# Kernel tuning notes

Measured on AMD Instinct MI355X. Metric: run time of the kernel, lower is better.

Reference implementation:

```python
import jax, jax.numpy as jnp
import numpy as np

NUM_EMB = 1024
EMB_DIM = 256
BETA = 0.25


def setup_inputs() -> dict:
    key = jax.random.key(0)
    k1, k2 = jax.random.split(key)
    z_e = jax.random.normal(k1, (32, EMB_DIM, 32, 32), dtype=jnp.float32)
    # original inits uniform(-1/num_emb, 1/num_emb)
    emb_weight = jax.random.uniform(k2, (NUM_EMB, EMB_DIM), dtype=jnp.float32,
                                    minval=-1.0 / NUM_EMB, maxval=1.0 / NUM_EMB)
    return {"z_e": z_e, "emb_weight": emb_weight}


def reference(z_e, emb_weight):
    # (B, C, H, W) -> (B, H, W, C)
    z = jnp.transpose(z_e, (0, 2, 3, 1))
    B, H, W, C = z.shape
    z_flat = z.reshape(-1, C)  # (N, C)
    # squared L2 distances to codebook: ||z||^2 + ||e||^2 - 2 z e^T
    d = (jnp.sum(z_flat ** 2, axis=1, keepdims=True)
         + jnp.sum(emb_weight ** 2, axis=1)
         - 2.0 * jnp.matmul(z_flat, emb_weight.T))  # (N, num_emb)
    encoding_indices = jnp.argmin(d, axis=1)  # (N,)
    # one-hot matmul == gather of codebook rows
    z_q = jnp.take(emb_weight, encoding_indices, axis=0).reshape(B, H, W, C)
    # vq losses
    L_e = jnp.mean((jax.lax.stop_gradient(z_q) - z) ** 2)
    L_q = jnp.mean((z_q - jax.lax.stop_gradient(z)) ** 2)
    vq_loss = L_e + BETA * L_q
    # straight-through estimator
    z_q_st = z + jax.lax.stop_gradient(z_q - z)
    z_q_out = jnp.transpose(z_q_st, (0, 3, 1, 2))  # (B, C, H, W)
    return z_q_out, vq_loss, encoding_indices
```

## Files before the change

kernel.cpp:

```cpp
#include <hip/hip_runtime.h>

#define NUM_EMB 1024
#define EMB_DIM 256
#define NPIX    32768
#define HW      1024
#define ZQ_ELEMS 8388608

#define WS_TNORM 8
#define WS_SNORM 8192
#define WS_KEYS  139264
#define WS_CNT   401408
#define WS_EB    403456

typedef unsigned long long u64;
typedef unsigned int u32;
typedef unsigned short u16;

typedef __bf16 bf16x8 __attribute__((ext_vector_type(8)));
typedef float f32x16 __attribute__((ext_vector_type(16)));
typedef u16 u16x8 __attribute__((ext_vector_type(8)));

__device__ __forceinline__ size_t eb_idx(int p, int g, int kt, int ks, int hi,
                                         int cl) {
  return ((((((size_t)p * 32 + g) * 8 + kt) * 2 + ks) * 2 + hi) * 32 + cl) * 8;
}

__device__ __forceinline__ float pw128_sq(const float* x, int stride) {
  float r[8];
#pragma unroll
  for (int j = 0; j < 8; ++j) {
    float v = x[(size_t)j * stride];
    r[j] = __fmul_rn(v, v);
  }
  for (int i = 8; i < 128; i += 8) {
#pragma unroll
    for (int j = 0; j < 8; ++j) {
      float v = x[(size_t)(i + j) * stride];
      r[j] = __fadd_rn(r[j], __fmul_rn(v, v));
    }
  }
  float s01 = __fadd_rn(r[0], r[1]);
  float s23 = __fadd_rn(r[2], r[3]);
  float s45 = __fadd_rn(r[4], r[5]);
  float s67 = __fadd_rn(r[6], r[7]);
  return __fadd_rn(__fadd_rn(s01, s23), __fadd_rn(s45, s67));
}

__device__ __forceinline__ void split3(float x, u16& h, u16& m, u16& l) {
  u32 u = __float_as_uint(x);
  u16 hb = (u16)((u + 0x7fffu + ((u >> 16) & 1u)) >> 16);
  float hf = __uint_as_float((u32)hb << 16);
  float r1 = x - hf;
  u32 u1 = __float_as_uint(r1);
  u16 mb = (u16)((u1 + 0x7fffu + ((u1 >> 16) & 1u)) >> 16);
  float mf = __uint_as_float((u32)mb << 16);
  float r2 = r1 - mf;
  u32 u2 = __float_as_uint(r2);
  u16 lb = (u16)((u2 + 0x7fffu + ((u2 >> 16) & 1u)) >> 16);
  h = hb; m = mb; l = lb;
}

__device__ __forceinline__ u64 shfl_xor_u64(u64 v, int msk) {
  const u32 lo = __shfl_xor((u32)v, msk, 64);
  const u32 hi = __shfl_xor((u32)(v >> 32), msk, 64);
  return ((u64)hi << 32) | lo;
}

__global__ __launch_bounds__(256) void vq_prep_kernel(
    const float* __restrict__ z, const float* __restrict__ emb,
    float* __restrict__ tnorm, float* __restrict__ snorm,
    u64* __restrict__ keys, double* __restrict__ loss_accum,
    u32* __restrict__ counter, u16* __restrict__ EB) {
  const int gid = blockIdx.x * 256 + threadIdx.x;
  if (gid == 0) *loss_accum = 0.0;
  if (gid == 1) *counter = 0u;
  if (gid < NPIX) {
    keys[gid] = ~0ull;
    const int b = gid >> 10, hw = gid & 1023;
    const float* base = z + (size_t)b * (EMB_DIM * HW) + hw;
    snorm[gid] = __fadd_rn(pw128_sq(base, HW), pw128_sq(base + (size_t)128 * HW, HW));
  } else {
    const int k = gid - NPIX;
    if (k < NUM_EMB) {
      const float* row = emb + (size_t)k * EMB_DIM;
      tnorm[k] = __fadd_rn(pw128_sq(row, 1), pw128_sq(row + 128, 1));
      const int g = k >> 5, cl = k & 31;
      for (int c = 0; c < EMB_DIM; c += 8) {
        u16x8 vh, vm, vl;
#pragma unroll
        for (int j = 0; j < 8; ++j) {
          u16 h_, m_, l_;
          split3(row[c + j], h_, m_, l_);
          vh[j] = h_; vm[j] = m_; vl[j] = l_;
        }
        const int kt = c >> 5, ks = (c >> 4) & 1, hi = (c >> 3) & 1;
        *(u16x8*)(EB + eb_idx(0, g, kt, ks, hi, cl)) = vh;
        *(u16x8*)(EB + eb_idx(1, g, kt, ks, hi, cl)) = vm;
        *(u16x8*)(EB + eb_idx(2, g, kt, ks, hi, cl)) = vl;
      }
    }
  }
}

__global__ __launch_bounds__(256, 2) void vq_main_kernel(
    const float* __restrict__ z, const u16* __restrict__ EB,
    const float* __restrict__ tnorm, const float* __restrict__ snorm,
    u64* __restrict__ keys) {
  __shared__ __align__(16) u16 zs[4][3][64][40];
  __shared__ u64 part[128][2];

  const int t   = threadIdx.x;
  const int hb  = blockIdx.x;
  const int bid = (hb & 7) * 256 + (hb >> 3);
  const int pt  = bid >> 3;
  const int ntb = bid & 7;
  const int m0  = pt * 128;
  const int n0  = ntb * 128;
  const int b   = m0 >> 10;
  const int hw0 = m0 & 1023;

  const int l    = t & 63;
  const int wid  = t >> 6;
  const int wpx0 = (wid >> 1) * 64;
  const int wcb  = (wid & 1) * 64;
  const int cl   = l & 31;
  const int hi   = l >> 5;
  const int gb   = ntb * 4 + (wid & 1) * 2;

  const int m_ = l & 31;
  const int h_ = l >> 5;
  const float* zcol = z + (size_t)b * (EMB_DIM * HW) + hw0 + wpx0 + 2 * m_;

  float2 gz[16];
  bf16x8 geA[3][2], geB[3][2];

  auto load_gz = [&](int kt) {
#pragma unroll
    for (int j = 0; j < 16; ++j)
      gz[j] = *(const float2*)(zcol + (size_t)(kt * 32 + h_ * 16 + j) * HW);
  };
  auto load_ge = [&](bf16x8 dst[3][2], int kt, int ks) {
#pragma unroll
    for (int p = 0; p < 3; ++p)
#pragma unroll
      for (int nn = 0; nn < 2; ++nn)
        dst[p][nn] = *(const bf16x8*)(EB + eb_idx(p, gb + nn, kt, ks, hi, cl));
  };
  auto stage = [&]() {
#pragma unroll
    for (int r = 0; r < 2; ++r) {
#pragma unroll
      for (int c = 0; c < 2; ++c) {
        u16x8 vh, vm, vl;
#pragma unroll
        for (int j = 0; j < 8; ++j) {
          const float x = r ? gz[c * 8 + j].y : gz[c * 8 + j].x;
          u16 h3, m3, l3;
          split3(x, h3, m3, l3);
          vh[j] = h3; vm[j] = m3; vl[j] = l3;
        }
        *(u16x8*)&zs[wid][0][2 * m_ + r][h_ * 16 + c * 8] = vh;
        *(u16x8*)&zs[wid][1][2 * m_ + r][h_ * 16 + c * 8] = vm;
        *(u16x8*)&zs[wid][2][2 * m_ + r][h_ * 16 + c * 8] = vl;
      }
    }
  };

  f32x16 acc[2][2];
#pragma unroll
  for (int i = 0; i < 2; ++i)
#pragma unroll
    for (int j = 0; j < 2; ++j)
#pragma unroll
      for (int r = 0; r < 16; ++r) acc[i][j][r] = 0.0f;

  load_gz(0);
  load_ge(geA, 0, 0);
  stage();
  load_gz(1);

  for (int kt = 0; kt < 8; ++kt) {
    load_ge(geB, kt, 1);
    {
      bf16x8 af[3][2];
#pragma unroll
      for (int p = 0; p < 3; ++p)
#pragma unroll
        for (int mt = 0; mt < 2; ++mt)
          af[p][mt] = *(const bf16x8*)&zs[wid][p][mt * 32 + cl][hi * 8];
#define PROD(PA, PB, GE)                                                      \
      _Pragma("unroll")                                                       \
      for (int mt = 0; mt < 2; ++mt) {                                        \
        _Pragma("unroll")                                                     \
        for (int nn = 0; nn < 2; ++nn)                                        \
          acc[mt][nn] = __builtin_amdgcn_mfma_f32_32x32x16_bf16(              \
              af[PA][mt], GE[PB][nn], acc[mt][nn], 0, 0, 0);                  \
      }
      PROD(0, 0, geA)
      PROD(0, 1, geA)
      PROD(1, 0, geA)
      PROD(1, 1, geA)
      PROD(0, 2, geA)
      PROD(2, 0, geA)
    }
    if (kt < 7) load_ge(geA, kt + 1, 0);
    {
      bf16x8 af[3][2];
#pragma unroll
      for (int p = 0; p < 3; ++p)
#pragma unroll
        for (int mt = 0; mt < 2; ++mt)
          af[p][mt] = *(const bf16x8*)&zs[wid][p][mt * 32 + cl][16 + hi * 8];
      PROD(0, 0, geB)
      PROD(0, 1, geB)
      PROD(1, 0, geB)
      PROD(1, 1, geB)
      PROD(0, 2, geB)
      PROD(2, 0, geB)
#undef PROD
    }
    if (kt < 7) {
      stage();
      if (kt < 6) load_gz(kt + 2);
    }
  }

  const float tv0 = tnorm[n0 + wcb + cl];
  const float tv1 = tnorm[n0 + wcb + 32 + cl];
  u64 bk[2][16];
#pragma unroll
  for (int mt = 0; mt < 2; ++mt)
#pragma unroll
    for (int reg = 0; reg < 16; ++reg) {
      const int row = wpx0 + mt * 32 + (reg & 3) + 8 * (reg >> 2) + 4 * hi;
      const float s = snorm[m0 + row];
      const float d0 = __fsub_rn(__fadd_rn(s, tv0), 2.0f * acc[mt][0][reg]);
      const float d1 = __fsub_rn(__fadd_rn(s, tv1), 2.0f * acc[mt][1][reg]);
      const u64 k0 = ((u64)__float_as_uint(d0) << 32) | (u32)(n0 + wcb + cl);
      const u64 k1 =
          ((u64)__float_as_uint(d1) << 32) | (u32)(n0 + wcb + 32 + cl);
      bk[mt][reg] = k0 < k1 ? k0 : k1;
    }
#pragma unroll
  for (int off = 1; off < 32; off <<= 1) {
#pragma unroll
    for (int mt = 0; mt < 2; ++mt)
#pragma unroll
      for (int reg = 0; reg < 16; ++reg) {
        const u64 o = shfl_xor_u64(bk[mt][reg], off);
        if (o < bk[mt][reg]) bk[mt][reg] = o;
      }
  }

  if (cl == 0) {
#pragma unroll
    for (int mt = 0; mt < 2; ++mt)
#pragma unroll
      for (int reg = 0; reg < 16; ++reg) {
        const int row = wpx0 + mt * 32 + (reg & 3) + 8 * (reg >> 2) + 4 * hi;
        part[row][wid & 1] = bk[mt][reg];
      }
  }
  __syncthreads();
  if (t < 128) {
    const u64 a = part[t][0], c = part[t][1];
    atomicMin(&keys[m0 + t], a < c ? a : c);
  }
}

__global__ __launch_bounds__(256) void vq_outputs_kernel(
    const float* __restrict__ z, const float* __restrict__ emb,
    const u64* __restrict__ keys, float* __restrict__ out,
    float* __restrict__ out_idx_f, double* __restrict__ loss_accum,
    u32* __restrict__ counter, float* __restrict__ out_loss) {
  const int t  = threadIdx.x;
  const int n0 = blockIdx.x * 64;
  const int m  = t & 63;
  const int c0 = t >> 6;
  const int b  = n0 >> 10;
  const int hw = n0 & 1023;
  const float* zb = z   + (size_t)b * (EMB_DIM * HW) + hw + m;
  float*       ob = out + (size_t)b * (EMB_DIM * HW) + hw + m;
  const int idx = (int)(u32)(keys[n0 + m] & 0xffffffffu);
  const float* er = emb + (size_t)idx * EMB_DIM;
  if (c0 == 0) out_idx_f[n0 + m] = (float)idx;

  double lsum = 0.0;
  for (int c = c0; c < EMB_DIM; c += 4) {
    const float e  = er[c];
    const float zv = zb[(size_t)c * HW];
    const float diff = e - zv;
    const float zq   = zv + diff;
    ob[(size_t)c * HW] = zq;
    lsum += (double)diff * (double)diff;
  }

  __shared__ double red[256];
  red[t] = lsum;
  __syncthreads();
  for (int s2 = 128; s2 > 0; s2 >>= 1) {
    if (t < s2) red[t] += red[t + s2];
    __syncthreads();
  }
  if (t == 0) {
    atomicAdd(loss_accum, red[0]);
    __threadfence();
    const u32 tick = atomicAdd(counter, 1u);
    if (tick == (u32)(NPIX / 64 - 1)) {
      const double total = atomicAdd(loss_accum, 0.0);
      const float L = (float)(total / (double)ZQ_ELEMS);
      out_loss[0] = __fadd_rn(L, __fmul_rn(0.25f, L));
    }
  }
}

extern "C" void kernel_launch(void* const* d_in, const int* in_sizes, int n_in,
                              void* d_out, int out_size, void* d_ws, size_t ws_size,
                              hipStream_t stream) {
  const float* z   = (const float*)d_in[0];
  const float* emb = (const float*)d_in[1];

  float* out       = (float*)d_out;
  float* out_loss  = out + ZQ_ELEMS;
  float* out_idx_f = out + ZQ_ELEMS + 1;

  double* loss_accum = (double*)d_ws;
  float*  tnorm = (float*)((char*)d_ws + WS_TNORM);
  float*  snorm = (float*)((char*)d_ws + WS_SNORM);
  u64*    keys  = (u64*)((char*)d_ws + WS_KEYS);
  u32*    counter = (u32*)((char*)d_ws + WS_CNT);
  u16*    EB    = (u16*)((char*)d_ws + WS_EB);

  vq_prep_kernel<<<132, 256, 0, stream>>>(z, emb, tnorm, snorm, keys, loss_accum,
                                          counter, EB);
  vq_main_kernel<<<2048, 256, 0, stream>>>(z, EB, tnorm, snorm, keys);
  vq_outputs_kernel<<<NPIX / 64, 256, 0, stream>>>(z, emb, keys, out, out_idx_f,
                                                   loss_accum, counter, out_loss);
}
```

Measured before the change: 204.5 us.

## Halve z staging granularity to raise occupancy to three blocks per CU

Restructures the main GEMM loop to run 16 half-steps of 16 channels instead of 8 steps of 32. This halves the register buffer of prefetched z values and the shared-memory staging tile. The launch bound rises from 2 to 3 blocks per CU so more waves can hide latency. The three-way bf16 split is inlined as explicit convert-and-subtract arithmetic. The cost is a finer-grained loop with more staging and shared-memory rounds, and possible register pressure or spills under the tighter occupancy bound.

```diff
diff --git a/kernel.cpp b/kernel.cpp
--- a/kernel.cpp
+++ b/kernel.cpp
@@ -102,11 +102,11 @@
   }
 }
 
-__global__ __launch_bounds__(256, 2) void vq_main_kernel(
+__global__ __launch_bounds__(256, 3) void vq_main_kernel(
     const float* __restrict__ z, const u16* __restrict__ EB,
     const float* __restrict__ tnorm, const float* __restrict__ snorm,
     u64* __restrict__ keys) {
-  __shared__ __align__(16) u16 zs[4][3][64][40];
+  __shared__ __align__(16) u16 zs[4][3][64][20];
   __shared__ u64 part[128][2];
 
   const int t   = threadIdx.x;
@@ -131,15 +131,16 @@
   const int h_ = l >> 5;
   const float* zcol = z + (size_t)b * (EMB_DIM * HW) + hw0 + wpx0 + 2 * m_;
 
-  float2 gz[16];
+  float2 gz[8];
   bf16x8 geA[3][2], geB[3][2];
 
-  auto load_gz = [&](int kt) {
-#pragma unroll
-    for (int j = 0; j < 16; ++j)
-      gz[j] = *(const float2*)(zcol + (size_t)(kt * 32 + h_ * 16 + j) * HW);
+  auto load_gz = [&](int s) {
+#pragma unroll
+    for (int j = 0; j < 8; ++j)
+      gz[j] = *(const float2*)(zcol + (size_t)(s * 16 + h_ * 8 + j) * HW);
   };
-  auto load_ge = [&](bf16x8 dst[3][2], int kt, int ks) {
+  auto load_ge = [&](bf16x8 dst[3][2], int s) {
+    const int kt = s >> 1, ks = s & 1;
 #pragma unroll
     for (int p = 0; p < 3; ++p)
 #pragma unroll
@@ -149,20 +150,21 @@
   auto stage = [&]() {
 #pragma unroll
     for (int r = 0; r < 2; ++r) {
-#pragma unroll
-      for (int c = 0; c < 2; ++c) {
-        u16x8 vh, vm, vl;
-#pragma unroll
-        for (int j = 0; j < 8; ++j) {
-          const float x = r ? gz[c * 8 + j].y : gz[c * 8 + j].x;
-          u16 h3, m3, l3;
-          split3(x, h3, m3, l3);
-          vh[j] = h3; vm[j] = m3; vl[j] = l3;
-        }
-        *(u16x8*)&zs[wid][0][2 * m_ + r][h_ * 16 + c * 8] = vh;
-        *(u16x8*)&zs[wid][1][2 * m_ + r][h_ * 16 + c * 8] = vm;
-        *(u16x8*)&zs[wid][2][2 * m_ + r][h_ * 16 + c * 8] = vl;
+      u16x8 vh, vm, vl;
+#pragma unroll
+      for (int j = 0; j < 8; ++j) {
+        const float x  = r ? gz[j].y : gz[j].x;
+        const float hf = (float)(__bf16)x;
+        const float r1 = x - hf;
+        const float mf = (float)(__bf16)r1;
+        const float r2 = r1 - mf;
+        vh[j] = (u16)(__float_as_uint(hf) >> 16);
+        vm[j] = (u16)(__float_as_uint(mf) >> 16);
+        vl[j] = (u16)(__float_as_uint((float)(__bf16)r2) >> 16);
       }
+      *(u16x8*)&zs[wid][0][2 * m_ + r][h_ * 8] = vh;
+      *(u16x8*)&zs[wid][1][2 * m_ + r][h_ * 8] = vm;
+      *(u16x8*)&zs[wid][2][2 * m_ + r][h_ * 8] = vl;
     }
   };
 
@@ -175,53 +177,38 @@
       for (int r = 0; r < 16; ++r) acc[i][j][r] = 0.0f;
 
   load_gz(0);
-  load_ge(geA, 0, 0);
+  load_ge(geA, 0);
   stage();
   load_gz(1);
 
-  for (int kt = 0; kt < 8; ++kt) {
-    load_ge(geB, kt, 1);
-    {
-      bf16x8 af[3][2];
-#pragma unroll
-      for (int p = 0; p < 3; ++p)
-#pragma unroll
-        for (int mt = 0; mt < 2; ++mt)
-          af[p][mt] = *(const bf16x8*)&zs[wid][p][mt * 32 + cl][hi * 8];
-#define PROD(PA, PB, GE)                                                      \
+  for (int s = 0; s < 16; ++s) {
+    bf16x8(&cur)[3][2] = (s & 1) ? geB : geA;
+    bf16x8(&nxt)[3][2] = (s & 1) ? geA : geB;
+    if (s < 15) load_ge(nxt, s + 1);
+    bf16x8 af[3][2];
+#pragma unroll
+    for (int p = 0; p < 3; ++p)
+#pragma unroll
+      for (int mt = 0; mt < 2; ++mt)
+        af[p][mt] = *(const bf16x8*)&zs[wid][p][mt * 32 + cl][hi * 8];
+#define PROD(PA, PB)                                                          \
+    _Pragma("unroll")                                                         \
+    for (int mt = 0; mt < 2; ++mt) {                                          \
       _Pragma("unroll")                                                       \
-      for (int mt = 0; mt < 2; ++mt) {                                        \
-        _Pragma("unroll")                                                     \
-        for (int nn = 0; nn < 2; ++nn)                                        \
-          acc[mt][nn] = __builtin_amdgcn_mfma_f32_32x32x16_bf16(              \
-              af[PA][mt], GE[PB][nn], acc[mt][nn], 0, 0, 0);                  \
-      }
-      PROD(0, 0, geA)
-      PROD(0, 1, geA)
-      PROD(1, 0, geA)
-      PROD(1, 1, geA)
-      PROD(0, 2, geA)
-      PROD(2, 0, geA)
-    }
-    if (kt < 7) load_ge(geA, kt + 1, 0);
-    {
-      bf16x8 af[3][2];
-#pragma unroll
-      for (int p = 0; p < 3; ++p)
-#pragma unroll
-        for (int mt = 0; mt < 2; ++mt)
-          af[p][mt] = *(const bf16x8*)&zs[wid][p][mt * 32 + cl][16 + hi * 8];
-      PROD(0, 0, geB)
-      PROD(0, 1, geB)
-      PROD(1, 0, geB)
-      PROD(1, 1, geB)
-      PROD(0, 2, geB)
-      PROD(2, 0, geB)
+      for (int nn = 0; nn < 2; ++nn)                                          \
+        acc[mt][nn] = __builtin_amdgcn_mfma_f32_32x32x16_bf16(                \
+            af[PA][mt], cur[PB][nn], acc[mt][nn], 0, 0, 0);                   \
+    }
+    PROD(0, 0)
+    PROD(0, 1)
+    PROD(1, 0)
+    PROD(1, 1)
+    PROD(0, 2)
+    PROD(2, 0)
 #undef PROD
-    }
-    if (kt < 7) {
+    if (s < 15) {
       stage();
-      if (kt < 6) load_gz(kt + 2);
+      if (s < 14) load_gz(s + 2);
     }
   }
 
```

New measurement: 204.9 us. Within noise of the previous version (+0.2%).
